# Kernel tuning notes

Measured on AMD Instinct MI355X. Metric: run time of the kernel, lower is better.

## Reference

```python
import jax, jax.numpy as jnp
import numpy as np
from math import sqrt

P_DROP = 0.2  # dropout_rate

def setup_inputs() -> dict:
    key = jax.random.key(0)
    ks = jax.random.split(key, 5)
    B, Cin, H, W = 32, 128, 64, 64
    Cout, kh, kw = 256, 3, 3
    k = sqrt(1.0 / (Cin * kh * kw))  # He-style init std from module
    x = jax.random.normal(ks[0], (B, Cin, H, W), dtype=jnp.float32)
    weight = jax.random.normal(ks[1], (Cout, Cin, kh, kw), dtype=jnp.float32) * k
    bias = jax.random.normal(ks[2], (Cout,), dtype=jnp.float32) * k
    # uniforms used for torch.rand(...) > p per batch element ('w' mode draws fresh masks per sample)
    u_w = jax.random.uniform(ks[3], (B, Cout, Cin, kh, kw), dtype=jnp.float32)
    u_b = jax.random.uniform(ks[4], (B, Cout), dtype=jnp.float32)
    return {"x": x, "weight": weight, "bias": bias, "u_w": u_w, "u_b": u_b}

def reference(x, weight, bias, u_w, u_b):
    # 'w' mode: per-sample dropped-out weight/bias, conv per sample -> vmapped batched conv.
    # Note: mask is (rand > p) with NO 1/(1-p) rescaling, matching the torch code.
    w_mask = (u_w > P_DROP).astype(weight.dtype)          # [B,O,I,kh,kw]
    b_mask = (u_b > P_DROP).astype(bias.dtype)            # [B,O]
    w_per = weight[None] * w_mask                          # [B,O,I,kh,kw]
    b_per = bias[None] * b_mask                            # [B,O]

    def conv_one(xi, wi):  # xi: [Cin,H,W], wi: [O,I,kh,kw]
        return jax.lax.conv_general_dilated(
            xi[None], wi,
            window_strides=(1, 1),
            padding=((1, 1), (1, 1)),
            dimension_numbers=("NCHW", "OIHW", "NCHW"),
        )[0]

    y = jax.vmap(conv_one)(x, w_per)                       # [B,O,H,W]
    return y + b_per[:, :, None, None]
```

## Files before the change

kernel.cpp:

```cpp
#include <hip/hip_runtime.h>
#include <cstdint>
#include <cstddef>

#define CIN   128
#define COUT  256
#define HW    64
#define NSP   4096
#define KTOT  1152
#define BATCH 32
#define PDROP 0.2f
#define LDT   40
#define WLD   1160

__device__ __forceinline__ unsigned short f2bf(float f) {
    unsigned int u = __builtin_bit_cast(unsigned int, f);
    u += 0x7fffu + ((u >> 16) & 1u);
    return (unsigned short)(u >> 16);
}

__device__ __align__(16) unsigned short g_zeros[64] = {0};

__device__ __forceinline__ void gl_lds16(const unsigned short* g, unsigned short* l) {
    __builtin_amdgcn_global_load_lds(
        (const __attribute__((address_space(1))) unsigned int*)g,
        (__attribute__((address_space(3))) unsigned int*)l,
        16, 0, 0);
}

__global__ __launch_bounds__(256) void prepass(
        const float* __restrict__ weight, const float* __restrict__ u_w,
        const float* __restrict__ x,
        unsigned short* __restrict__ wt2, unsigned short* __restrict__ xt)
{
    __shared__ __align__(16) unsigned char smem[16 * WLD * 2];
    const int t256 = threadIdx.x;

    if (blockIdx.x < 512) {
        unsigned short* tile16 = reinterpret_cast<unsigned short*>(smem);
        const int wb  = blockIdx.x;
        const int b   = wb >> 4;
        const int mb  = (wb >> 3) & 1;
        const int wm2 = (wb >> 2) & 1;
        const int mi  = wb & 3;
        const int obase = mb * 128 + wm2 * 64 + mi * 16;

        const float* wsrc = weight + (size_t)obase * KTOT;
        const float* usrc = u_w + (size_t)(b * COUT + obase) * KTOT;
        #pragma unroll
        for (int j = 0; j < 18; ++j) {
            const int f4 = j * 256 + t256;
            const float4 wv = reinterpret_cast<const float4*>(wsrc)[f4];
            const float4 uv = reinterpret_cast<const float4*>(usrc)[f4];
            const float w4[4] = {wv.x, wv.y, wv.z, wv.w};
            const float u4[4] = {uv.x, uv.y, uv.z, uv.w};
            #pragma unroll
            for (int e = 0; e < 4; ++e) {
                const int fl  = f4 * 4 + e;
                const int row = fl / KTOT;
                const int ks  = fl - row * KTOT;
                const int i   = ks / 9;
                const int r   = ks - 9 * i;
                tile16[row * WLD + r * CIN + i] =
                    f2bf((u4[e] > PDROP) ? w4[e] : 0.f);
            }
        }
        __syncthreads();

        const size_t blk16 = ((size_t)(b * 2 + mb)) * 18432;
        #pragma unroll
        for (int s = 0; s < 9; ++s) {
            const int g     = s * 256 + t256;
            const int run   = g >> 6;
            const int inner = g & 63;
            const int slab  = run >= 18;
            const int rr    = run - slab * 18;
            const int tap   = rr >> 1;
            const int ki    = rr & 1;
            const int q     = inner >> 4;
            const int il15  = inner & 15;
            const uint4 v = *reinterpret_cast<const uint4*>(
                &tile16[il15 * WLD + tap * CIN + slab * 64 + ki * 32 + q * 8]);
            const size_t dst16 = blk16
                + (size_t)(((slab * 9 + tap) * 2 + ki) * 2 + wm2) * 256
                + mi * 64 + inner;
            *reinterpret_cast<uint4*>(wt2 + dst16 * 8) = v;
        }
    } else {
        unsigned int* shp = reinterpret_cast<unsigned int*>(smem);
        const int bidx = blockIdx.x - 512;
        const int b    = bidx >> 6;
        const int hw0  = (bidx & 63) * 64;
        const int ib   = t256 >> 4;
        const int hw4  = (t256 & 15) * 4;
        #pragma unroll
        for (int j = 0; j < 4; ++j) {
            const int p = ib + 16 * j;
            const float4 v0 = *reinterpret_cast<const float4*>(
                x + ((size_t)(b * CIN + 2 * p)) * NSP + hw0 + hw4);
            const float4 v1 = *reinterpret_cast<const float4*>(
                x + ((size_t)(b * CIN + 2 * p + 1)) * NSP + hw0 + hw4);
            const float e0[4] = {v0.x, v0.y, v0.z, v0.w};
            const float e1[4] = {v1.x, v1.y, v1.z, v1.w};
            #pragma unroll
            for (int c = 0; c < 4; ++c) {
                const unsigned int val =
                    (unsigned int)f2bf(e0[c]) | ((unsigned int)f2bf(e1[c]) << 16);
                shp[(hw4 + c) * 65 + p] = val;
            }
        }
        __syncthreads();
        #pragma unroll
        for (int j = 0; j < 4; ++j) {
            const int idx  = j * 256 + t256;
            const int row  = idx >> 4;
            const int part = idx & 15;
            uint4 v;
            v.x = shp[row * 65 + part * 4 + 0];
            v.y = shp[row * 65 + part * 4 + 1];
            v.z = shp[row * 65 + part * 4 + 2];
            v.w = shp[row * 65 + part * 4 + 3];
            *reinterpret_cast<uint4*>(
                xt + ((size_t)(b * NSP + hw0 + row)) * CIN + part * 8) = v;
        }
    }
}

__global__ __launch_bounds__(256, 3) void conv_v8(
        const unsigned short* __restrict__ wt2,
        const unsigned short* __restrict__ xt,
        const float* __restrict__ bias, const float* __restrict__ u_b,
        float* __restrict__ out)
{
    using frag  = __attribute__((ext_vector_type(8))) short;
    using f32x4 = __attribute__((ext_vector_type(4))) float;

    __shared__ unsigned short Xs[4 * 66 * 64];

    const int tid  = threadIdx.x;
    const int lane = tid & 63;
    const int q    = lane >> 4;
    const int l15  = lane & 15;
    const int wv   = tid >> 6;
    const int wm   = (wv >> 1) * 64;
    const int wn   = (wv & 1) * 64;
    const int wnrow = wn >> 6;
    const int wm2  = wv >> 1;

    const int f   = blockIdx.x + 32 * blockIdx.y + 64 * blockIdx.z;
    const int wid = (f & 7) * 256 + (f >> 3);
    const int b   = wid >> 6;
    const int m0  = ((wid >> 5) & 1) * 128;
    const int n0  = (wid & 31) * 128;
    const int mb  = m0 >> 7;
    const int ph0 = n0 >> 6;

    const unsigned short* xtb = xt + (size_t)b * NSP * CIN;

    const unsigned short* gA2[4];
    {
        const unsigned short* base = wt2
            + (size_t)(b * 2 + mb) * 147456 + wm2 * 2048 + lane * 8;
        #pragma unroll
        for (int mi = 0; mi < 4; ++mi) gA2[mi] = base + mi * 512;
    }

    const int kcl = (lane & 7) ^ ((1 + (lane >> 3)) & 7);
    const int xsrc_lane = (lane >> 3) * CIN + kcl * 8;
    const int hhx = ph0 - 1 + wv;
    const bool vrow = ((unsigned)hhx < 64u);
    unsigned short* const xdst = &Xs[(wv * 66 + 1) * 64];

    int xoff[4];
    #pragma unroll
    for (int ni = 0; ni < 4; ++ni) xoff[ni] = (ni * 16 + l15 + 1) * 64;
    int xr[3][2];
    #pragma unroll
    for (int dxi = 0; dxi < 3; ++dxi)
        #pragma unroll
        for (int ki = 0; ki < 2; ++ki)
            xr[dxi][ki] = ((ki * 4 + q) ^ ((l15 + dxi) & 7)) * 8;

    f32x4 acc[4][4];
    #pragma unroll
    for (int i = 0; i < 4; ++i)
        #pragma unroll
        for (int j = 0; j < 4; ++j)
            acc[i][j] = (f32x4){0.f, 0.f, 0.f, 0.f};

    {
        const int cell = tid >> 5;
        const int rr   = cell >> 1;
        const int cc   = (cell & 1) ? 65 : 0;
        *reinterpret_cast<unsigned int*>(
            &Xs[(rr * 66 + cc) * 64 + (tid & 31) * 2]) = 0u;
    }

    auto stage_x = [&](int i0) {
        const unsigned short* sx = vrow
            ? xtb + (size_t)hhx * HW * CIN + i0 + xsrc_lane
            : g_zeros;
        #pragma unroll
        for (int g = 0; g < 8; ++g)
            gl_lds16(vrow ? (sx + g * 8 * CIN) : sx, xdst + g * 512);
    };

    auto loadB = [&](int pp, frag* dst) {
        const int tap = pp >> 1;
        const int ki  = pp & 1;
        const int dy  = tap / 3 - 1;
        const int dx  = tap - 3 * (tap / 3) - 1;
        const int dxi = dx + 1;
        const int cb  = (wnrow + dy + 1) * 4224 + dx * 64;
        #pragma unroll
        for (int ni = 0; ni < 4; ++ni)
            dst[ni] = *reinterpret_cast<const frag*>(
                &Xs[cb + xoff[ni] + xr[dxi][ki]]);
    };

    #pragma unroll
    for (int s2 = 0; s2 < 2; ++s2) {
        const int sofs = s2 * 73728;

        if (s2) __syncthreads();

        frag afr[3][4];
        #pragma unroll
        for (int mi = 0; mi < 4; ++mi) {
            afr[0][mi] = *reinterpret_cast<const frag*>(gA2[mi] + sofs);
            afr[1][mi] = *reinterpret_cast<const frag*>(gA2[mi] + sofs + 4096);
        }

        stage_x(s2 * 64);
        __syncthreads();

        frag bring[2][4];
        loadB(0, bring[0]);

        #pragma unroll
        for (int p = 0; p < 18; ++p) {
            if (p + 2 < 18) {
                const int np   = p + 2;
                const int noff = sofs + (np >> 1) * 8192 + (np & 1) * 4096;
                #pragma unroll
                for (int mi = 0; mi < 4; ++mi)
                    afr[(p + 2) % 3][mi] =
                        *reinterpret_cast<const frag*>(gA2[mi] + noff);
            }
            if (p + 1 < 18) loadB(p + 1, bring[(p + 1) & 1]);

            __builtin_amdgcn_s_setprio(1);
            #pragma unroll
            for (int mi = 0; mi < 4; ++mi)
                #pragma unroll
                for (int ni = 0; ni < 4; ++ni)
                    acc[mi][ni] = __builtin_amdgcn_mfma_f32_16x16x32_bf16(
                        afr[p % 3][mi], bring[p & 1][ni], acc[mi][ni], 0, 0, 0);
            __builtin_amdgcn_s_setprio(0);
        }
    }

    float* ob = out + (size_t)b * COUT * NSP;
    #pragma unroll
    for (int mi = 0; mi < 4; ++mi) {
        #pragma unroll
        for (int rg = 0; rg < 4; ++rg) {
            const int o  = m0 + wm + mi * 16 + q * 4 + rg;
            const float bvv = (u_b[b * COUT + o] > PDROP) ? bias[o] : 0.f;
            float* orow = ob + (size_t)o * NSP + n0 + wn + l15;
            #pragma unroll
            for (int ni = 0; ni < 4; ++ni)
                orow[ni * 16] = acc[mi][ni][rg] + bvv;
        }
    }
}

__global__ __launch_bounds__(256) void conv_fb(
        const float* __restrict__ x, const float* __restrict__ weight,
        const float* __restrict__ bias, const float* __restrict__ u_w,
        const float* __restrict__ u_b, float* __restrict__ out)
{
    using frag  = __attribute__((ext_vector_type(8))) short;
    using f32x4 = __attribute__((ext_vector_type(4))) float;

    __shared__ unsigned short As[128 * LDT];
    __shared__ unsigned short Bs[128 * LDT];

    const int tid  = threadIdx.x;
    const int lane = tid & 63;
    const int q    = lane >> 4;
    const int l15  = lane & 15;
    const int wv   = tid >> 6;
    const int wm   = (wv >> 1) * 64;
    const int wn   = (wv & 1) * 64;

    const int b  = blockIdx.z;
    const int m0 = blockIdx.y * 128;
    const int n0 = blockIdx.x * 128;

    const int arow = tid >> 1;
    const int acol = (tid & 1) * 16;
    const int pn = tid & 127;
    const int kh = (tid >> 7) * 16;
    const int p  = n0 + pn;
    const int ph = p >> 6;
    const int pw = p & 63;

    const float* xb = x + (size_t)b * CIN * NSP;

    f32x4 acc[4][4];
    #pragma unroll
    for (int i = 0; i < 4; ++i)
        #pragma unroll
        for (int j = 0; j < 4; ++j)
            acc[i][j] = (f32x4){0.f, 0.f, 0.f, 0.f};

    const int a_rd = (wm + l15) * LDT + q * 8;
    const int b_rd = (wn + l15) * LDT + q * 8;

    for (int s = 0; s < 36; ++s) {
        const int r  = s >> 2;
        const int i0 = (s & 3) * 32;

        float aw[16], au[16];
        {
            const float* wsrc = weight + (size_t)(m0 + arow) * KTOT;
            const float* usrc = u_w + (size_t)(b * COUT + m0 + arow) * KTOT;
            #pragma unroll
            for (int ii = 0; ii < 16; ++ii) {
                const int kk = (i0 + acol + ii) * 9 + r;
                aw[ii] = wsrc[kk];
                au[ii] = usrc[kk];
            }
        }

        const int hh = ph + (r / 3) - 1;
        const int ww = pw + (r % 3) - 1;
        float bx[16];
        #pragma unroll
        for (int j = 0; j < 16; ++j) bx[j] = 0.f;
        if (((unsigned)hh < 64u) && ((unsigned)ww < 64u)) {
            const float* xsrc = xb + (size_t)(i0 + kh) * NSP + hh * HW + ww;
            #pragma unroll
            for (int j = 0; j < 16; ++j) bx[j] = xsrc[(size_t)j * NSP];
        }

        __syncthreads();

        {
            union { unsigned short u16[16]; uint4 v[2]; } tu;
            #pragma unroll
            for (int ii = 0; ii < 16; ++ii)
                tu.u16[ii] = f2bf((au[ii] > PDROP) ? aw[ii] : 0.f);
            uint4* d = reinterpret_cast<uint4*>(&As[arow * LDT + acol]);
            d[0] = tu.v[0]; d[1] = tu.v[1];
        }
        {
            union { unsigned short u16[16]; uint4 v[2]; } tu;
            #pragma unroll
            for (int j = 0; j < 16; ++j) tu.u16[j] = f2bf(bx[j]);
            uint4* d = reinterpret_cast<uint4*>(&Bs[pn * LDT + kh]);
            d[0] = tu.v[0]; d[1] = tu.v[1];
        }

        __syncthreads();

        frag af[4], bfr[4];
        #pragma unroll
        for (int mi = 0; mi < 4; ++mi)
            af[mi] = *reinterpret_cast<const frag*>(&As[a_rd + mi * 16 * LDT]);
        #pragma unroll
        for (int ni = 0; ni < 4; ++ni)
            bfr[ni] = *reinterpret_cast<const frag*>(&Bs[b_rd + ni * 16 * LDT]);
        #pragma unroll
        for (int mi = 0; mi < 4; ++mi)
            #pragma unroll
            for (int ni = 0; ni < 4; ++ni)
                acc[mi][ni] = __builtin_amdgcn_mfma_f32_16x16x32_bf16(
                    af[mi], bfr[ni], acc[mi][ni], 0, 0, 0);
    }

    float* ob = out + (size_t)b * COUT * NSP;
    #pragma unroll
    for (int mi = 0; mi < 4; ++mi) {
        #pragma unroll
        for (int rg = 0; rg < 4; ++rg) {
            const int o = m0 + wm + mi * 16 + q * 4 + rg;
            const float bvv = (u_b[b * COUT + o] > PDROP) ? bias[o] : 0.f;
            float* orow = ob + (size_t)o * NSP + n0 + wn + l15;
            #pragma unroll
            for (int ni = 0; ni < 4; ++ni)
                orow[ni * 16] = acc[mi][ni][rg] + bvv;
        }
    }
}

extern "C" void kernel_launch(void* const* d_in, const int* in_sizes, int n_in,
                              void* d_out, int out_size, void* d_ws, size_t ws_size,
                              hipStream_t stream)
{
    const float* x      = (const float*)d_in[0];
    const float* weight = (const float*)d_in[1];
    const float* bias   = (const float*)d_in[2];
    const float* u_w    = (const float*)d_in[3];
    const float* u_b    = (const float*)d_in[4];
    float* out = (float*)d_out;

    const size_t wt_bytes = (size_t)BATCH * COUT * KTOT * sizeof(unsigned short);
    const size_t xt_bytes = (size_t)BATCH * NSP * CIN * sizeof(unsigned short);
    dim3 grid(NSP / 128, COUT / 128, BATCH);

    if (ws_size >= wt_bytes + xt_bytes) {
        unsigned short* wtp = (unsigned short*)d_ws;
        unsigned short* xtp = (unsigned short*)((char*)d_ws + wt_bytes);
        prepass<<<512 + 2048, 256, 0, stream>>>(weight, u_w, x, wtp, xtp);
        conv_v8<<<grid, 256, 0, stream>>>(wtp, xtp, bias, u_b, out);
    } else {
        conv_fb<<<grid, 256, 0, stream>>>(x, weight, bias, u_w, u_b, out);
    }
}
```

Baseline: 279.0 us.

## Switch conv main loop to 32x32x16 bf16 MFMA with matching weight layout

Replaces the 16x16x32 MFMA tiling (4x4 fragments per wave) with 32x32x16 MFMA (2x2 fragments per wave). The prepass weight-fragment layout, the LDS swizzled B-fragment addressing and the output epilogue row mapping are rewritten to match. The larger MFMA shape cuts the number of A and B fragment loads per FLOP and the instruction count, at the cost of a longer K loop (36 steps) with less per-step prefetch depth for B.

```diff
diff --git a/kernel.cpp b/kernel.cpp
--- a/kernel.cpp
+++ b/kernel.cpp
@@ -41,8 +41,9 @@
         const int b   = wb >> 4;
         const int mb  = (wb >> 3) & 1;
         const int wm2 = (wb >> 2) & 1;
-        const int mi  = wb & 3;
-        const int obase = mb * 128 + wm2 * 64 + mi * 16;
+        const int mi  = (wb >> 1) & 1;
+        const int h   = wb & 1;
+        const int obase = mb * 128 + wm2 * 64 + mi * 32 + h * 16;
 
         const float* wsrc = weight + (size_t)obase * KTOT;
         const float* usrc = u_w + (size_t)(b * COUT + obase) * KTOT;
@@ -66,23 +67,23 @@
         }
         __syncthreads();
 
-        const size_t blk16 = ((size_t)(b * 2 + mb)) * 18432;
-        #pragma unroll
-        for (int s = 0; s < 9; ++s) {
-            const int g     = s * 256 + t256;
-            const int run   = g >> 6;
-            const int inner = g & 63;
-            const int slab  = run >= 18;
-            const int rr    = run - slab * 18;
-            const int tap   = rr >> 1;
-            const int ki    = rr & 1;
-            const int q     = inner >> 4;
-            const int il15  = inner & 15;
+        const size_t blkbase = ((size_t)(b * 2 + mb)) * 18432;
+        #pragma unroll
+        for (int j = 0; j < 9; ++j) {
+            const int g    = j * 256 + t256;
+            const int c    = g >> 5;
+            const int slot = g & 31;
+            const int lsub = slot & 15;
+            const int lhi2 = slot >> 4;
+            const int lane = lhi2 * 32 + h * 16 + lsub;
+            const int slab = c / 36;
+            const int rem  = c - slab * 36;
+            const int tap  = rem >> 2;
+            const int ks   = rem & 3;
             const uint4 v = *reinterpret_cast<const uint4*>(
-                &tile16[il15 * WLD + tap * CIN + slab * 64 + ki * 32 + q * 8]);
-            const size_t dst16 = blk16
-                + (size_t)(((slab * 9 + tap) * 2 + ki) * 2 + wm2) * 256
-                + mi * 64 + inner;
+                &tile16[lsub * WLD + tap * CIN + slab * 64 + ks * 16 + lhi2 * 8]);
+            const int chunk = (((slab * 9 + tap) * 4 + ks) * 2 + wm2) * 2 + mi;
+            const size_t dst16 = blkbase + (size_t)chunk * 64 + lane;
             *reinterpret_cast<uint4*>(wt2 + dst16 * 8) = v;
         }
     } else {
@@ -125,26 +126,26 @@
     }
 }
 
-__global__ __launch_bounds__(256, 3) void conv_v8(
+__global__ __launch_bounds__(256, 3) void conv_v9(
         const unsigned short* __restrict__ wt2,
         const unsigned short* __restrict__ xt,
         const float* __restrict__ bias, const float* __restrict__ u_b,
         float* __restrict__ out)
 {
-    using frag  = __attribute__((ext_vector_type(8))) short;
-    using f32x4 = __attribute__((ext_vector_type(4))) float;
+    using frag   = __attribute__((ext_vector_type(8))) short;
+    using f32x16 = __attribute__((ext_vector_type(16))) float;
 
     __shared__ unsigned short Xs[4 * 66 * 64];
 
     const int tid  = threadIdx.x;
     const int lane = tid & 63;
-    const int q    = lane >> 4;
-    const int l15  = lane & 15;
+    const int l31  = lane & 31;
+    const int lhi  = lane >> 5;
     const int wv   = tid >> 6;
-    const int wm   = (wv >> 1) * 64;
+    const int wm2  = wv >> 1;
+    const int wm   = wm2 * 64;
     const int wn   = (wv & 1) * 64;
     const int wnrow = wn >> 6;
-    const int wm2  = wv >> 1;
 
     const int f   = blockIdx.x + 32 * blockIdx.y + 64 * blockIdx.z;
     const int wid = (f & 7) * 256 + (f >> 3);
@@ -156,12 +157,12 @@
 
     const unsigned short* xtb = xt + (size_t)b * NSP * CIN;
 
-    const unsigned short* gA2[4];
+    const unsigned short* gA32[2];
     {
         const unsigned short* base = wt2
-            + (size_t)(b * 2 + mb) * 147456 + wm2 * 2048 + lane * 8;
-        #pragma unroll
-        for (int mi = 0; mi < 4; ++mi) gA2[mi] = base + mi * 512;
+            + (size_t)(b * 2 + mb) * 147456 + wm2 * 1024 + lane * 8;
+        gA32[0] = base;
+        gA32[1] = base + 512;
     }
 
     const int kcl = (lane & 7) ^ ((1 + (lane >> 3)) & 7);
@@ -170,22 +171,24 @@
     const bool vrow = ((unsigned)hhx < 64u);
     unsigned short* const xdst = &Xs[(wv * 66 + 1) * 64];
 
-    int xoff[4];
-    #pragma unroll
-    for (int ni = 0; ni < 4; ++ni) xoff[ni] = (ni * 16 + l15 + 1) * 64;
-    int xr[3][2];
-    #pragma unroll
-    for (int dxi = 0; dxi < 3; ++dxi)
-        #pragma unroll
-        for (int ki = 0; ki < 2; ++ki)
-            xr[dxi][ki] = ((ki * 4 + q) ^ ((l15 + dxi) & 7)) * 8;
-
-    f32x4 acc[4][4];
-    #pragma unroll
-    for (int i = 0; i < 4; ++i)
-        #pragma unroll
-        for (int j = 0; j < 4; ++j)
-            acc[i][j] = (f32x4){0.f, 0.f, 0.f, 0.f};
+    int bcol[2][3];
+    int sw[3];
+    #pragma unroll
+    for (int dxi = 0; dxi < 3; ++dxi) {
+        sw[dxi] = (l31 + dxi) & 7;
+        #pragma unroll
+        for (int ni = 0; ni < 2; ++ni)
+            bcol[ni][dxi] = (ni * 32 + l31 + dxi) * 64;
+    }
+
+    f32x16 acc2[2][2];
+    #pragma unroll
+    for (int mi = 0; mi < 2; ++mi)
+        #pragma unroll
+        for (int ni = 0; ni < 2; ++ni)
+            #pragma unroll
+            for (int r = 0; r < 16; ++r)
+                acc2[mi][ni][r] = 0.f;
 
     {
         const int cell = tid >> 5;
@@ -204,72 +207,71 @@
             gl_lds16(vrow ? (sx + g * 8 * CIN) : sx, xdst + g * 512);
     };
 
-    auto loadB = [&](int pp, frag* dst) {
-        const int tap = pp >> 1;
-        const int ki  = pp & 1;
-        const int dy  = tap / 3 - 1;
-        const int dx  = tap - 3 * (tap / 3) - 1;
-        const int dxi = dx + 1;
-        const int cb  = (wnrow + dy + 1) * 4224 + dx * 64;
-        #pragma unroll
-        for (int ni = 0; ni < 4; ++ni)
-            dst[ni] = *reinterpret_cast<const frag*>(
-                &Xs[cb + xoff[ni] + xr[dxi][ki]]);
-    };
-
     #pragma unroll
     for (int s2 = 0; s2 < 2; ++s2) {
         const int sofs = s2 * 73728;
 
         if (s2) __syncthreads();
 
-        frag afr[3][4];
-        #pragma unroll
-        for (int mi = 0; mi < 4; ++mi) {
-            afr[0][mi] = *reinterpret_cast<const frag*>(gA2[mi] + sofs);
-            afr[1][mi] = *reinterpret_cast<const frag*>(gA2[mi] + sofs + 4096);
+        frag afr[4][2];
+        #pragma unroll
+        for (int k0 = 0; k0 < 3; ++k0) {
+            const int off = sofs + (k0 >> 2) * 8192 + (k0 & 3) * 2048;
+            #pragma unroll
+            for (int mi = 0; mi < 2; ++mi)
+                afr[k0][mi] = *reinterpret_cast<const frag*>(gA32[mi] + off);
         }
 
         stage_x(s2 * 64);
         __syncthreads();
 
-        frag bring[2][4];
-        loadB(0, bring[0]);
-
-        #pragma unroll
-        for (int p = 0; p < 18; ++p) {
-            if (p + 2 < 18) {
-                const int np   = p + 2;
-                const int noff = sofs + (np >> 1) * 8192 + (np & 1) * 4096;
+        #pragma unroll
+        for (int kl = 0; kl < 36; ++kl) {
+            if (kl + 3 < 36) {
+                const int nk  = kl + 3;
+                const int off = sofs + (nk >> 2) * 8192 + (nk & 3) * 2048;
                 #pragma unroll
-                for (int mi = 0; mi < 4; ++mi)
-                    afr[(p + 2) % 3][mi] =
-                        *reinterpret_cast<const frag*>(gA2[mi] + noff);
+                for (int mi = 0; mi < 2; ++mi)
+                    afr[nk & 3][mi] =
+                        *reinterpret_cast<const frag*>(gA32[mi] + off);
             }
-            if (p + 1 < 18) loadB(p + 1, bring[(p + 1) & 1]);
+            const int tap = kl >> 2;
+            const int ks  = kl & 3;
+            const int dy  = tap / 3 - 1;
+            const int dx  = tap - 3 * (tap / 3) - 1;
+            const int dxi = dx + 1;
+            const int cb  = (wnrow + dy + 1) * 4224;
+            const int k8  = ks * 2 + lhi;
+
+            frag bfr[2];
+            #pragma unroll
+            for (int ni = 0; ni < 2; ++ni)
+                bfr[ni] = *reinterpret_cast<const frag*>(
+                    &Xs[cb + bcol[ni][dxi] + ((k8 ^ sw[dxi]) << 3)]);
 
             __builtin_amdgcn_s_setprio(1);
             #pragma unroll
-            for (int mi = 0; mi < 4; ++mi)
+            for (int mi = 0; mi < 2; ++mi)
                 #pragma unroll
-                for (int ni = 0; ni < 4; ++ni)
-                    acc[mi][ni] = __builtin_amdgcn_mfma_f32_16x16x32_bf16(
-                        afr[p % 3][mi], bring[p & 1][ni], acc[mi][ni], 0, 0, 0);
+                for (int ni = 0; ni < 2; ++ni)
+                    acc2[mi][ni] = __builtin_amdgcn_mfma_f32_32x32x16_bf16(
+                        afr[kl & 3][mi], bfr[ni], acc2[mi][ni], 0, 0, 0);
             __builtin_amdgcn_s_setprio(0);
         }
     }
 
     float* ob = out + (size_t)b * COUT * NSP;
     #pragma unroll
-    for (int mi = 0; mi < 4; ++mi) {
-        #pragma unroll
-        for (int rg = 0; rg < 4; ++rg) {
-            const int o  = m0 + wm + mi * 16 + q * 4 + rg;
+    for (int mi = 0; mi < 2; ++mi) {
+        #pragma unroll
+        for (int r = 0; r < 16; ++r) {
+            const int row = (r & 3) + 8 * (r >> 2) + 4 * lhi;
+            const int o   = m0 + wm + mi * 32 + row;
             const float bvv = (u_b[b * COUT + o] > PDROP) ? bias[o] : 0.f;
-            float* orow = ob + (size_t)o * NSP + n0 + wn + l15;
-            #pragma unroll
-            for (int ni = 0; ni < 4; ++ni)
-                orow[ni * 16] = acc[mi][ni][rg] + bvv;
+            float* orow = ob + (size_t)o * NSP + n0 + wn + l31;
+            #pragma unroll
+            for (int ni = 0; ni < 2; ++ni)
+                orow[ni * 32] = acc2[mi][ni][r] + bvv;
         }
     }
 }
@@ -413,7 +415,7 @@
         unsigned short* wtp = (unsigned short*)d_ws;
         unsigned short* xtp = (unsigned short*)((char*)d_ws + wt_bytes);
         prepass<<<512 + 2048, 256, 0, stream>>>(weight, u_w, x, wtp, xtp);
-        conv_v8<<<grid, 256, 0, stream>>>(wtp, xtp, bias, u_b, out);
+        conv_v9<<<grid, 256, 0, stream>>>(wtp, xtp, bias, u_b, out);
     } else {
         conv_fb<<<grid, 256, 0, stream>>>(x, weight, bias, u_w, u_b, out);
     }
```

Measured after the change: 288.8 us. 3.5% more time.
